# Optimization experiments

Measured on AMD Instinct MI355X. Metric: run time of the kernel, lower is better.

Reference implementation:

```python
import jax, jax.numpy as jnp
import numpy as np

B, S, U = 64, 64, 16
EMB = 10
D = U - 2 + 2 * EMB      # encoder d_model = 34
DD = 3                   # decoder d_model
FF = 4                   # dim_feedforward
NL = 4                   # num layers (enc and dec)
ENH = 2                  # encoder heads
WV, SV = 10000, 400      # word / syllable vocab sizes


def _ln(x, w, b, eps=1e-5):
    mu = jnp.mean(x, -1, keepdims=True)
    var = jnp.mean((x - mu) ** 2, -1, keepdims=True)
    return (x - mu) / jnp.sqrt(var + eps) * w + b


def _mha(xq, xkv, qkv_w, qkv_b, out_w, out_b, nhead, mask=None):
    d = xq.shape[-1]
    wq, wk, wv = jnp.split(qkv_w, 3, axis=0)
    bq, bk, bv = jnp.split(qkv_b, 3, axis=0)
    q = xq @ wq.T + bq
    k = xkv @ wk.T + bk
    v = xkv @ wv.T + bv
    b_, sq, sk = q.shape[0], q.shape[1], k.shape[1]
    dh = d // nhead
    q = q.reshape(b_, sq, nhead, dh)
    k = k.reshape(b_, sk, nhead, dh)
    v = v.reshape(b_, sk, nhead, dh)
    scores = jnp.einsum('bqhd,bkhd->bhqk', q, k) * (1.0 / np.sqrt(dh))
    if mask is not None:
        scores = scores + mask
    attn = jax.nn.softmax(scores, axis=-1)
    out = jnp.einsum('bhqk,bkhd->bqhd', attn, v).reshape(b_, sq, d)
    return out @ out_w.T + out_b


def _pos_encoding(batch, d_model):
    # Faithful to the original quirk: pe has shape [max_len, 1, d] and is added
    # to a batch-first [B,S,D] tensor as x + pe[:B]  ->  row b of pe is added
    # to ALL sequence positions of batch element b.
    pos = jnp.arange(batch, dtype=jnp.float32)[:, None]
    div = jnp.exp(jnp.arange(0, d_model, 2, dtype=jnp.float32) * (-np.log(10000.0) / d_model))
    ang = pos * div  # [B, D/2]
    pe = jnp.stack([jnp.sin(ang), jnp.cos(ang)], axis=-1).reshape(batch, d_model)
    return pe[:, None, :]  # [B,1,D]


def setup_inputs() -> dict:
    key = jax.random.key(0)
    ks = iter(jax.random.split(key, 64))

    def n(shape, s=0.1):
        return jax.random.normal(next(ks), shape, dtype=jnp.float32) * s

    base = jax.random.uniform(next(ks), (B, S, U), dtype=jnp.float32)
    widx = jax.random.randint(next(ks), (B, S), 0, WV).astype(jnp.float32)
    sidx = jax.random.randint(next(ks), (B, S), 0, SV).astype(jnp.float32)
    src = base.at[:, :, U - 2].set(widx).at[:, :, U - 1].set(sidx)
    return {
        'src': src,
        'word_emb': jax.random.uniform(next(ks), (WV, EMB), jnp.float32, -0.1, 0.1),
        'syll_emb': jax.random.uniform(next(ks), (SV, EMB), jnp.float32, -0.1, 0.1),
        'enc_qkv_w': n((NL, 3 * D, D)), 'enc_qkv_b': jnp.zeros((NL, 3 * D)),
        'enc_out_w': n((NL, D, D)), 'enc_out_b': jnp.zeros((NL, D)),
        'enc_ln1_w': jnp.ones((NL, D)), 'enc_ln1_b': jnp.zeros((NL, D)),
        'enc_lin1_w': n((NL, FF, D)), 'enc_lin1_b': jnp.zeros((NL, FF)),
        'enc_lin2_w': n((NL, D, FF)), 'enc_lin2_b': jnp.zeros((NL, D)),
        'enc_ln2_w': jnp.ones((NL, D)), 'enc_ln2_b': jnp.zeros((NL, D)),
        'norm_w': jnp.ones((D,)), 'norm_b': jnp.zeros((D,)),
        'eo_w': jax.random.uniform(next(ks), (DD, D), jnp.float32, -0.1, 0.1),
        'eo_b': jnp.zeros((DD,)),
        'dec_sa_qkv_w': n((NL, 3 * DD, DD)), 'dec_sa_qkv_b': jnp.zeros((NL, 3 * DD)),
        'dec_sa_out_w': n((NL, DD, DD)), 'dec_sa_out_b': jnp.zeros((NL, DD)),
        'dec_ln1_w': jnp.ones((NL, DD)), 'dec_ln1_b': jnp.zeros((NL, DD)),
        'dec_ca_qkv_w': n((NL, 3 * DD, DD)), 'dec_ca_qkv_b': jnp.zeros((NL, 3 * DD)),
        'dec_ca_out_w': n((NL, DD, DD)), 'dec_ca_out_b': jnp.zeros((NL, DD)),
        'dec_ln2_w': jnp.ones((NL, DD)), 'dec_ln2_b': jnp.zeros((NL, DD)),
        'dec_lin1_w': n((NL, FF, DD)), 'dec_lin1_b': jnp.zeros((NL, FF)),
        'dec_lin2_w': n((NL, DD, FF)), 'dec_lin2_b': jnp.zeros((NL, DD)),
        'dec_ln3_w': jnp.ones((NL, DD)), 'dec_ln3_b': jnp.zeros((NL, DD)),
    }


def reference(src, word_emb, syll_emb,
              enc_qkv_w, enc_qkv_b, enc_out_w, enc_out_b,
              enc_ln1_w, enc_ln1_b, enc_lin1_w, enc_lin1_b,
              enc_lin2_w, enc_lin2_b, enc_ln2_w, enc_ln2_b,
              norm_w, norm_b, eo_w, eo_b,
              dec_sa_qkv_w, dec_sa_qkv_b, dec_sa_out_w, dec_sa_out_b,
              dec_ln1_w, dec_ln1_b,
              dec_ca_qkv_w, dec_ca_qkv_b, dec_ca_out_w, dec_ca_out_b,
              dec_ln2_w, dec_ln2_b,
              dec_lin1_w, dec_lin1_b, dec_lin2_w, dec_lin2_b,
              dec_ln3_w, dec_ln3_b):
    b, s = src.shape[0], src.shape[1]
    # embed_lyrics
    widx = src[:, :, U - 2].astype(jnp.int32)
    sidx = src[:, :, U - 1].astype(jnp.int32)
    x = jnp.concatenate([src[:, :, :U - 2], word_emb[widx], syll_emb[sidx]], axis=2)  # [B,S,D]
    x = x + _pos_encoding(b, D)
    # TransformerEncoder (post-norm, relu, dropout=0) + final LayerNorm
    for l in range(NL):
        sa = _mha(x, x, enc_qkv_w[l], enc_qkv_b[l], enc_out_w[l], enc_out_b[l], ENH)
        x = _ln(x + sa, enc_ln1_w[l], enc_ln1_b[l])
        ff = jax.nn.relu(x @ enc_lin1_w[l].T + enc_lin1_b[l]) @ enc_lin2_w[l].T + enc_lin2_b[l]
        x = _ln(x + ff, enc_ln2_w[l], enc_ln2_b[l])
    x = _ln(x, norm_w, norm_b)
    memory = x @ eo_w.T + eo_b  # [B,S,3]

    causal = jnp.where(jnp.tril(jnp.ones((s, s), bool)), 0.0, -1e9).astype(jnp.float32)

    def decode(tgt):
        y = tgt
        for l in range(NL):
            sa = _mha(y, y, dec_sa_qkv_w[l], dec_sa_qkv_b[l], dec_sa_out_w[l], dec_sa_out_b[l], 1, causal)
            y = _ln(y + sa, dec_ln1_w[l], dec_ln1_b[l])
            ca = _mha(y, memory, dec_ca_qkv_w[l], dec_ca_qkv_b[l], dec_ca_out_w[l], dec_ca_out_b[l], 1)
            y = _ln(y + ca, dec_ln2_w[l], dec_ln2_b[l])
            ff = jax.nn.relu(y @ dec_lin1_w[l].T + dec_lin1_b[l]) @ dec_lin2_w[l].T + dec_lin2_b[l]
            y = _ln(y + ff, dec_ln3_w[l], dec_ln3_b[l])
        return y

    # mask, position i only depends on tgt[:, :i+1], so a fixed-size padded
    # buffer + scan computes identical values.
    def step(tgt, i):
        out_i = jax.lax.dynamic_slice_in_dim(decode(tgt), i, 1, axis=1)  # [B,1,3]
        return jax.lax.dynamic_update_slice(tgt, out_i, (0, i + 1, 0)), None

    tgt0 = jnp.zeros((b, s, DD), jnp.float32)
    tgt, _ = jax.lax.scan(step, tgt0, jnp.arange(s - 1))
    return jnp.concatenate([tgt, src[:, :, U - 2:U - 1], src[:, :, U - 1:U]], axis=2)
```

## Files before the change

kernel.cpp:

```cpp
#include <hip/hip_runtime.h>
#include <math.h>

#define B_ 64
#define S_ 64
#define U_ 16
#define EMB_ 10
#define D_ 34
#define DD_ 3
#define FF_ 4
#define NL_ 4

typedef float v2f __attribute__((ext_vector_type(2)));

__global__ __launch_bounds__(512) void enc_kernel(
    const float* __restrict__ src, const float* __restrict__ wemb,
    const float* __restrict__ semb,
    const float* __restrict__ qkv_w, const float* __restrict__ qkv_b,
    const float* __restrict__ out_w, const float* __restrict__ out_b,
    const float* __restrict__ ln1_w, const float* __restrict__ ln1_b,
    const float* __restrict__ lin1_w, const float* __restrict__ lin1_b,
    const float* __restrict__ lin2_w, const float* __restrict__ lin2_b,
    const float* __restrict__ ln2_w, const float* __restrict__ ln2_b,
    const float* __restrict__ norm_w, const float* __restrict__ norm_b,
    const float* __restrict__ eo_w, const float* __restrict__ eo_b,
    float* __restrict__ mem, float* __restrict__ out)
{
    const int b = blockIdx.x;
    const int tid = threadIdx.x;
    const int wv_ = tid >> 6;
    const int lane = tid & 63;

    __shared__ float xs[S_][D_ + 1];
    __shared__ float tmp[S_][D_ + 1];
    __shared__ float att[S_][D_ + 1];
    __shared__ __align__(16) float qsh[2][S_][21];
    __shared__ __align__(16) float ksh[2][S_][20];
    __shared__ __align__(16) float vsh[2][S_][20];
    __shared__ float ffh[S_][5];
    __shared__ float pacc[4][128][19];

    const float rs17 = 0.24253562503633297f;
    const float negln = -logf(10000.0f) / (float)D_;

    #pragma unroll
    for (int rr = 0; rr < 5; ++rr) {
        int idx = tid + rr * 512;
        if (idx < S_ * D_) {
            int pos = idx / D_, d = idx % D_;
            float v;
            if (d < U_ - 2) {
                v = src[(b * S_ + pos) * U_ + d];
            } else if (d < U_ - 2 + EMB_) {
                int wi = (int)src[(b * S_ + pos) * U_ + (U_ - 2)];
                v = wemb[wi * EMB_ + (d - (U_ - 2))];
            } else {
                int si = (int)src[(b * S_ + pos) * U_ + (U_ - 1)];
                v = semb[si * EMB_ + (d - (U_ - 2 + EMB_))];
            }
            int k = d >> 1;
            float div = __expf((float)(2 * k) * negln);
            float ang = (float)b * div;
            v += (d & 1) ? __cosf(ang) : __sinf(ang);
            xs[pos][d] = v;
        }
    }
    __syncthreads();

    for (int l = 0; l < NL_; ++l) {
        const float* Wq = qkv_w + l * 3 * D_ * D_;
        const float* Bq = qkv_b + l * 3 * D_;

        {
            v2f xr2[17];
            #pragma unroll
            for (int d2 = 0; d2 < 17; ++d2) {
                v2f t; t.x = xs[lane][2 * d2]; t.y = xs[lane][2 * d2 + 1];
                xr2[d2] = t;
            }
            #pragma unroll
            for (int rb = 0; rb < 13; ++rb) {
                int r = wv_ + (rb << 3);
                if (r < 3 * D_) {
                    int ru = __builtin_amdgcn_readfirstlane(r);
                    const v2f* w2 = (const v2f*)(Wq + ru * D_);
                    v2f a2; a2.x = Bq[ru]; a2.y = 0.f;
                    #pragma unroll
                    for (int d2 = 0; d2 < 17; ++d2)
                        a2 = __builtin_elementwise_fma(xr2[d2], w2[d2], a2);
                    float acc = a2.x + a2.y;
                    if (ru < D_)          { int h = (ru >= 17), dd = ru - h * 17; qsh[h][lane][dd] = acc; }
                    else if (ru < 2 * D_) { int rr2 = ru - D_;     int h = (rr2 >= 17), dd = rr2 - h * 17; ksh[h][lane][dd] = acc; }
                    else                  { int rr2 = ru - 2 * D_; int h = (rr2 >= 17), dd = rr2 - h * 17; vsh[h][lane][dd] = acc; }
                }
            }
        }
        __syncthreads();

        {
            int c = tid >> 7, hq = tid & 127;
            int h = hq >> 6, qi = hq & 63;
            float qv[17], acc[17];
            #pragma unroll
            for (int d = 0; d < 17; ++d) { qv[d] = qsh[h][qi][d]; acc[d] = 0.f; }
            float ssum = 0.f;
            int j0 = c * 16;
            #pragma unroll 4
            for (int jj = 0; jj < 16; ++jj) {
                int j = j0 + jj;
                const float4* kr = (const float4*)ksh[h][j];
                const float4* vr = (const float4*)vsh[h][j];
                float4 k0 = kr[0], k1 = kr[1], k2 = kr[2], k3 = kr[3];
                float  k16 = ksh[h][j][16];
                float4 v0 = vr[0], v1 = vr[1], v2 = vr[2], v3 = vr[3];
                float  v16 = vsh[h][j][16];
                float sE = qv[0]*k0.x + qv[2]*k0.z + qv[4]*k1.x + qv[6]*k1.z +
                           qv[8]*k2.x + qv[10]*k2.z + qv[12]*k3.x + qv[14]*k3.z;
                float sO = qv[1]*k0.y + qv[3]*k0.w + qv[5]*k1.y + qv[7]*k1.w +
                           qv[9]*k2.y + qv[11]*k2.w + qv[13]*k3.y + qv[15]*k3.w;
                float sc = sE + sO + qv[16]*k16;
                float e = __expf(sc * rs17);
                ssum += e;
                acc[0] += e*v0.x;  acc[1] += e*v0.y;  acc[2] += e*v0.z;  acc[3] += e*v0.w;
                acc[4] += e*v1.x;  acc[5] += e*v1.y;  acc[6] += e*v1.z;  acc[7] += e*v1.w;
                acc[8] += e*v2.x;  acc[9] += e*v2.y;  acc[10] += e*v2.z; acc[11] += e*v2.w;
                acc[12] += e*v3.x; acc[13] += e*v3.y; acc[14] += e*v3.z; acc[15] += e*v3.w;
                acc[16] += e*v16;
            }
            #pragma unroll
            for (int d = 0; d < 17; ++d) pacc[c][hq][d] = acc[d];
            pacc[c][hq][17] = ssum;
        }
        __syncthreads();

        if (tid < 128) {
            int h = tid >> 6, qi = tid & 63;
            int off = h * 17;
            float ssum = pacc[0][tid][17] + pacc[1][tid][17] +
                         pacc[2][tid][17] + pacc[3][tid][17];
            float inv = 1.f / ssum;
            #pragma unroll
            for (int d = 0; d < 17; ++d)
                att[qi][off + d] = (pacc[0][tid][d] + pacc[1][tid][d] +
                                    pacc[2][tid][d] + pacc[3][tid][d]) * inv;
        }
        __syncthreads();

        {
            v2f ar2[17];
            #pragma unroll
            for (int d2 = 0; d2 < 17; ++d2) {
                v2f t; t.x = att[lane][2 * d2]; t.y = att[lane][2 * d2 + 1];
                ar2[d2] = t;
            }
            const float* Wo = out_w + l * D_ * D_;
            const float* Bo = out_b + l * D_;
            #pragma unroll
            for (int rb = 0; rb < 5; ++rb) {
                int d = wv_ + (rb << 3);
                if (d < D_) {
                    int du = __builtin_amdgcn_readfirstlane(d);
                    const v2f* w2 = (const v2f*)(Wo + du * D_);
                    v2f a2; a2.x = Bo[du]; a2.y = 0.f;
                    #pragma unroll
                    for (int d2 = 0; d2 < 17; ++d2)
                        a2 = __builtin_elementwise_fma(ar2[d2], w2[d2], a2);
                    tmp[lane][du] = xs[lane][du] + a2.x + a2.y;
                }
            }
        }
        __syncthreads();

        {
            int row = tid >> 3, sub = tid & 7;
            float s = 0.f, sq = 0.f;
            #pragma unroll
            for (int d = sub; d < D_; d += 8) { float t = tmp[row][d]; s += t; sq = fmaf(t, t, sq); }
            #pragma unroll
            for (int m = 1; m < 8; m <<= 1) { s += __shfl_xor(s, m, 8); sq += __shfl_xor(sq, m, 8); }
            float mu = s * (1.0f / D_);
            float var = fmaf(sq, 1.0f / D_, -mu * mu);
            float rstd = rsqrtf(var + 1e-5f);
            #pragma unroll
            for (int d = sub; d < D_; d += 8)
                xs[row][d] = (tmp[row][d] - mu) * rstd * ln1_w[l * D_ + d] + ln1_b[l * D_ + d];
        }
        __syncthreads();

        if (wv_ < 4) {
            int fu = __builtin_amdgcn_readfirstlane(wv_);
            const v2f* w2 = (const v2f*)(lin1_w + l * FF_ * D_ + fu * D_);
            v2f a2; a2.x = lin1_b[l * FF_ + fu]; a2.y = 0.f;
            #pragma unroll
            for (int d2 = 0; d2 < 17; ++d2) {
                v2f t; t.x = xs[lane][2 * d2]; t.y = xs[lane][2 * d2 + 1];
                a2 = __builtin_elementwise_fma(t, w2[d2], a2);
            }
            ffh[lane][fu] = fmaxf(a2.x + a2.y, 0.f);
        }
        __syncthreads();

        {
            float h0 = ffh[lane][0], h1 = ffh[lane][1],
                  h2 = ffh[lane][2], h3 = ffh[lane][3];
            const float* W2 = lin2_w + l * D_ * FF_;
            const float* B2 = lin2_b + l * D_;
            #pragma unroll
            for (int rb = 0; rb < 5; ++rb) {
                int d = wv_ + (rb << 3);
                if (d < D_) {
                    int du = __builtin_amdgcn_readfirstlane(d);
                    const float* wrow = W2 + du * FF_;
                    float acc = fmaf(h0, wrow[0], fmaf(h1, wrow[1],
                                fmaf(h2, wrow[2], fmaf(h3, wrow[3], B2[du]))));
                    tmp[lane][du] = xs[lane][du] + acc;
                }
            }
        }
        __syncthreads();

        {
            int row = tid >> 3, sub = tid & 7;
            float s = 0.f, sq = 0.f;
            #pragma unroll
            for (int d = sub; d < D_; d += 8) { float t = tmp[row][d]; s += t; sq = fmaf(t, t, sq); }
            #pragma unroll
            for (int m = 1; m < 8; m <<= 1) { s += __shfl_xor(s, m, 8); sq += __shfl_xor(sq, m, 8); }
            float mu = s * (1.0f / D_);
            float var = fmaf(sq, 1.0f / D_, -mu * mu);
            float rstd = rsqrtf(var + 1e-5f);
            #pragma unroll
            for (int d = sub; d < D_; d += 8)
                xs[row][d] = (tmp[row][d] - mu) * rstd * ln2_w[l * D_ + d] + ln2_b[l * D_ + d];
        }
        __syncthreads();
    }

    {
        int row = tid >> 3, sub = tid & 7;
        float s = 0.f, sq = 0.f;
        #pragma unroll
        for (int d = sub; d < D_; d += 8) { float t = xs[row][d]; s += t; sq = fmaf(t, t, sq); }
        #pragma unroll
        for (int m = 1; m < 8; m <<= 1) { s += __shfl_xor(s, m, 8); sq += __shfl_xor(sq, m, 8); }
        float mu = s * (1.0f / D_);
        float var = fmaf(sq, 1.0f / D_, -mu * mu);
        float rstd = rsqrtf(var + 1e-5f);
        #pragma unroll
        for (int d = sub; d < D_; d += 8)
            tmp[row][d] = (xs[row][d] - mu) * rstd * norm_w[d] + norm_b[d];
    }
    __syncthreads();

    if (wv_ < 3) {
        int ru = __builtin_amdgcn_readfirstlane(wv_);
        const v2f* w2 = (const v2f*)(eo_w + ru * D_);
        v2f a2; a2.x = eo_b[ru]; a2.y = 0.f;
        #pragma unroll
        for (int d2 = 0; d2 < 17; ++d2) {
            v2f t; t.x = tmp[lane][2 * d2]; t.y = tmp[lane][2 * d2 + 1];
            a2 = __builtin_elementwise_fma(t, w2[d2], a2);
        }
        mem[(b * S_ + lane) * DD_ + ru] = a2.x + a2.y;
    }

    if (tid < S_) {
        out[(b * S_ + tid) * 5 + 3] = src[(b * S_ + tid) * U_ + (U_ - 2)];
        out[(b * S_ + tid) * 5 + 4] = src[(b * S_ + tid) * U_ + (U_ - 1)];
    }
}

#define PIN(x) asm volatile("" : "+v"(x))

template <int CTRL>
__device__ __forceinline__ float dpp_add(float v) {
    int t = __builtin_amdgcn_update_dpp(0, __float_as_int(v), CTRL, 0xf, 0xf, true);
    return v + __int_as_float(t);
}

__device__ __forceinline__ float wave_sum_l63(float v) {
    v = dpp_add<0x111>(v);
    v = dpp_add<0x112>(v);
    v = dpp_add<0x114>(v);
    v = dpp_add<0x118>(v);
    v = dpp_add<0x142>(v);
    v = dpp_add<0x143>(v);
    return v;
}

__device__ __forceinline__ float bcast63(float v) {
    return __int_as_float(__builtin_amdgcn_readlane(__float_as_int(v), 63));
}

__device__ __forceinline__ void ln3e(float z0, float z1, float z2,
                                     float w0, float w1, float w2,
                                     float b0, float b1, float b2,
                                     float& o0, float& o1, float& o2) {
    float s1 = (z0 + z1) + z2;
    float s2 = fmaf(z0, z0, fmaf(z1, z1, z2 * z2));
    float mu = s1 * (1.0f / 3.0f);
    float vpe = fmaf(s2, (1.0f / 3.0f), fmaf(-mu, mu, 1e-5f));
    float rstd = __builtin_amdgcn_rsqf(vpe);
    o0 = fmaf(z0 - mu, rstd * w0, b0);
    o1 = fmaf(z1 - mu, rstd * w1, b1);
    o2 = fmaf(z2 - mu, rstd * w2, b2);
}

__global__ __launch_bounds__(64, 1) void dec_kernel(
    const float* __restrict__ mem,
    const float* __restrict__ sa_qkv_w, const float* __restrict__ sa_qkv_b,
    const float* __restrict__ sa_out_w, const float* __restrict__ sa_out_b,
    const float* __restrict__ gln1_w, const float* __restrict__ gln1_b,
    const float* __restrict__ ca_qkv_w, const float* __restrict__ ca_qkv_b,
    const float* __restrict__ ca_out_w, const float* __restrict__ ca_out_b,
    const float* __restrict__ gln2_w, const float* __restrict__ gln2_b,
    const float* __restrict__ l1_w, const float* __restrict__ l1_b,
    const float* __restrict__ l2_w, const float* __restrict__ l2_b,
    const float* __restrict__ gln3_w, const float* __restrict__ gln3_b,
    float* __restrict__ out)
{
    const int b = blockIdx.x;
    const int lane = threadIdx.x;
    const float LOG2E = 1.4426950408889634f;
    const float rs3 = 0.5773502691896258f;
    const float QS = rs3 * LOG2E;

    __shared__ __align__(16) float fst[NL_][40];
    for (int t = lane; t < NL_ * 40; t += 64) {
        int l = t / 40, s = t % 40;
        float v = 0.f;
        if      (s < 12) v = l1_w[l * 12 + s];
        else if (s < 16) v = l1_b[l * 4 + (s - 12)];
        else if (s < 28) v = l2_w[l * 12 + (s - 16)];
        else if (s < 31) v = l2_b[l * 3 + (s - 28)];
        else if (s < 34) v = gln3_w[l * 3 + (s - 31)];
        else if (s < 37) v = gln3_b[l * 3 + (s - 34)];
        fst[l][s] = v;
    }
    __syncthreads();

    float Wsq[NL_][9][3], Bsq[NL_][9];
    float Wso[NL_][3][3], Bso[NL_][3];
    float N1w[NL_][3], N1b[NL_][3];
    float Wcq[NL_][3][3], Bcq[NL_][3];
    float Wco[NL_][3][3], Bco[NL_][3];
    float N2w[NL_][3], N2b[NL_][3];

    #pragma unroll
    for (int l = 0; l < NL_; ++l) {
        #pragma unroll
        for (int r = 0; r < 9; ++r) {
            float sc = (r < 3) ? QS : 1.0f;
            Bsq[l][r] = sa_qkv_b[l * 9 + r] * sc;
            #pragma unroll
            for (int c = 0; c < 3; ++c) Wsq[l][r][c] = sa_qkv_w[l * 27 + r * 3 + c] * sc;
        }
        #pragma unroll
        for (int r = 0; r < 3; ++r) {
            Bso[l][r] = sa_out_b[l * 3 + r];
            Bcq[l][r] = ca_qkv_b[l * 9 + r] * QS;
            Bco[l][r] = ca_out_b[l * 3 + r];
            N1w[l][r] = gln1_w[l * 3 + r];  N1b[l][r] = gln1_b[l * 3 + r];
            N2w[l][r] = gln2_w[l * 3 + r];  N2b[l][r] = gln2_b[l * 3 + r];
            #pragma unroll
            for (int c = 0; c < 3; ++c) {
                Wso[l][r][c] = sa_out_w[l * 9 + r * 3 + c];
                Wcq[l][r][c] = ca_qkv_w[l * 27 + r * 3 + c] * QS;
                Wco[l][r][c] = ca_out_w[l * 9 + r * 3 + c];
            }
        }
    }

    float m0 = mem[(b * S_ + lane) * DD_ + 0];
    float m1 = mem[(b * S_ + lane) * DD_ + 1];
    float m2 = mem[(b * S_ + lane) * DD_ + 2];

    float ck[NL_][3], cv[NL_][3];
    #pragma unroll
    for (int l = 0; l < NL_; ++l) {
        #pragma unroll
        for (int r = 0; r < 3; ++r) {
            ck[l][r] = ca_qkv_w[l * 27 + (3 + r) * 3 + 0] * m0 +
                       ca_qkv_w[l * 27 + (3 + r) * 3 + 1] * m1 +
                       ca_qkv_w[l * 27 + (3 + r) * 3 + 2] * m2 + ca_qkv_b[l * 9 + 3 + r];
            cv[l][r] = ca_qkv_w[l * 27 + (6 + r) * 3 + 0] * m0 +
                       ca_qkv_w[l * 27 + (6 + r) * 3 + 1] * m1 +
                       ca_qkv_w[l * 27 + (6 + r) * 3 + 2] * m2 + ca_qkv_b[l * 9 + 6 + r];
        }
    }

    #pragma unroll
    for (int l = 0; l < NL_; ++l) {
        #pragma unroll
        for (int r = 0; r < 9; ++r) {
            PIN(Bsq[l][r]);
            #pragma unroll
            for (int c = 0; c < 3; ++c) PIN(Wsq[l][r][c]);
        }
        #pragma unroll
        for (int r = 0; r < 3; ++r) {
            PIN(Bso[l][r]); PIN(Bcq[l][r]); PIN(Bco[l][r]);
            PIN(N1w[l][r]); PIN(N1b[l][r]); PIN(N2w[l][r]); PIN(N2b[l][r]);
            #pragma unroll
            for (int c = 0; c < 3; ++c) { PIN(Wso[l][r][c]); PIN(Wcq[l][r][c]); PIN(Wco[l][r][c]); }
        }
    }

    float sk[NL_][3] = {{0.f}}, sv[NL_][3] = {{0.f}};

    if (lane < 3) out[(b * S_ + 0) * 5 + lane] = 0.f;

    float y0 = 0.f, y1 = 0.f, y2 = 0.f;

    for (int i = 0; i < S_ - 1; ++i) {
        float msa = (lane <= i) ? 0.f : -1.0e30f;
        #pragma unroll
        for (int l = 0; l < NL_; ++l) {
            float wv[40];
            {
                const float4* fp = (const float4*)fst[l];
                #pragma unroll
                for (int k = 0; k < 10; ++k) {
                    float4 t4 = fp[k];
                    wv[4 * k + 0] = t4.x; wv[4 * k + 1] = t4.y;
                    wv[4 * k + 2] = t4.z; wv[4 * k + 3] = t4.w;
                }
                #pragma unroll
                for (int k = 0; k < 37; ++k) PIN(wv[k]);
            }

            float q[3], kn[3], vn[3];
            #pragma unroll
            for (int r = 0; r < 3; ++r) {
                q[r]  = fmaf(Wsq[l][r][0], y0, fmaf(Wsq[l][r][1], y1, fmaf(Wsq[l][r][2], y2, Bsq[l][r])));
                kn[r] = fmaf(Wsq[l][3 + r][0], y0, fmaf(Wsq[l][3 + r][1], y1, fmaf(Wsq[l][3 + r][2], y2, Bsq[l][3 + r])));
                vn[r] = fmaf(Wsq[l][6 + r][0], y0, fmaf(Wsq[l][6 + r][1], y1, fmaf(Wsq[l][6 + r][2], y2, Bsq[l][6 + r])));
            }
            if (lane == i) {
                #pragma unroll
                for (int r = 0; r < 3; ++r) { sk[l][r] = kn[r]; sv[l][r] = vn[r]; }
            }
            float sc = fmaf(q[0], sk[l][0], fmaf(q[1], sk[l][1], fmaf(q[2], sk[l][2], msa)));
            float e = __builtin_amdgcn_exp2f(sc);
            float es  = wave_sum_l63(e);
            float ev0 = wave_sum_l63(e * sv[l][0]);
            float ev1 = wave_sum_l63(e * sv[l][1]);
            float ev2 = wave_sum_l63(e * sv[l][2]);
            float inv = __builtin_amdgcn_rcpf(bcast63(es));
            float a0 = bcast63(ev0) * inv, a1 = bcast63(ev1) * inv, a2 = bcast63(ev2) * inv;
            float s0 = fmaf(Wso[l][0][0], a0, fmaf(Wso[l][0][1], a1, fmaf(Wso[l][0][2], a2, Bso[l][0])));
            float s1 = fmaf(Wso[l][1][0], a0, fmaf(Wso[l][1][1], a1, fmaf(Wso[l][1][2], a2, Bso[l][1])));
            float s2 = fmaf(Wso[l][2][0], a0, fmaf(Wso[l][2][1], a1, fmaf(Wso[l][2][2], a2, Bso[l][2])));
            ln3e(y0 + s0, y1 + s1, y2 + s2,
                 N1w[l][0], N1w[l][1], N1w[l][2], N1b[l][0], N1b[l][1], N1b[l][2],
                 y0, y1, y2);

            float p0 = fmaf(Wcq[l][0][0], y0, fmaf(Wcq[l][0][1], y1, fmaf(Wcq[l][0][2], y2, Bcq[l][0])));
            float p1 = fmaf(Wcq[l][1][0], y0, fmaf(Wcq[l][1][1], y1, fmaf(Wcq[l][1][2], y2, Bcq[l][1])));
            float p2 = fmaf(Wcq[l][2][0], y0, fmaf(Wcq[l][2][1], y1, fmaf(Wcq[l][2][2], y2, Bcq[l][2])));
            float sc2 = fmaf(p0, ck[l][0], fmaf(p1, ck[l][1], p2 * ck[l][2]));
            float e2 = __builtin_amdgcn_exp2f(sc2);
            float cs  = wave_sum_l63(e2);
            float cw0 = wave_sum_l63(e2 * cv[l][0]);
            float cw1 = wave_sum_l63(e2 * cv[l][1]);
            float cw2 = wave_sum_l63(e2 * cv[l][2]);
            inv = __builtin_amdgcn_rcpf(bcast63(cs));
            a0 = bcast63(cw0) * inv; a1 = bcast63(cw1) * inv; a2 = bcast63(cw2) * inv;
            float c0 = fmaf(Wco[l][0][0], a0, fmaf(Wco[l][0][1], a1, fmaf(Wco[l][0][2], a2, Bco[l][0])));
            float c1 = fmaf(Wco[l][1][0], a0, fmaf(Wco[l][1][1], a1, fmaf(Wco[l][1][2], a2, Bco[l][1])));
            float c2 = fmaf(Wco[l][2][0], a0, fmaf(Wco[l][2][1], a1, fmaf(Wco[l][2][2], a2, Bco[l][2])));
            ln3e(y0 + c0, y1 + c1, y2 + c2,
                 N2w[l][0], N2w[l][1], N2w[l][2], N2b[l][0], N2b[l][1], N2b[l][2],
                 y0, y1, y2);

            float h0 = fmaxf(fmaf(wv[0], y0, fmaf(wv[1],  y1, fmaf(wv[2],  y2, wv[12]))), 0.f);
            float h1 = fmaxf(fmaf(wv[3], y0, fmaf(wv[4],  y1, fmaf(wv[5],  y2, wv[13]))), 0.f);
            float h2 = fmaxf(fmaf(wv[6], y0, fmaf(wv[7],  y1, fmaf(wv[8],  y2, wv[14]))), 0.f);
            float h3 = fmaxf(fmaf(wv[9], y0, fmaf(wv[10], y1, fmaf(wv[11], y2, wv[15]))), 0.f);
            float f0 = fmaf(wv[16], h0, fmaf(wv[17], h1, fmaf(wv[18], h2, fmaf(wv[19], h3, wv[28]))));
            float f1 = fmaf(wv[20], h0, fmaf(wv[21], h1, fmaf(wv[22], h2, fmaf(wv[23], h3, wv[29]))));
            float f2 = fmaf(wv[24], h0, fmaf(wv[25], h1, fmaf(wv[26], h2, fmaf(wv[27], h3, wv[30]))));
            ln3e(y0 + f0, y1 + f1, y2 + f2,
                 wv[31], wv[32], wv[33], wv[34], wv[35], wv[36],
                 y0, y1, y2);
        }
        if (lane == 0) {
            out[(b * S_ + i + 1) * 5 + 0] = y0;
            out[(b * S_ + i + 1) * 5 + 1] = y1;
            out[(b * S_ + i + 1) * 5 + 2] = y2;
        }
    }
}

extern "C" void kernel_launch(void* const* d_in, const int* in_sizes, int n_in,
                              void* d_out, int out_size, void* d_ws, size_t ws_size,
                              hipStream_t stream) {
    const float* src  = (const float*)d_in[0];
    const float* wemb = (const float*)d_in[1];
    const float* semb = (const float*)d_in[2];

    float* mem = (float*)d_ws;
    float* out = (float*)d_out;

    enc_kernel<<<B_, 512, 0, stream>>>(
        src, wemb, semb,
        (const float*)d_in[3],  (const float*)d_in[4],
        (const float*)d_in[5],  (const float*)d_in[6],
        (const float*)d_in[7],  (const float*)d_in[8],
        (const float*)d_in[9],  (const float*)d_in[10],
        (const float*)d_in[11], (const float*)d_in[12],
        (const float*)d_in[13], (const float*)d_in[14],
        (const float*)d_in[15], (const float*)d_in[16],
        (const float*)d_in[17], (const float*)d_in[18],
        mem, out);

    dec_kernel<<<B_, 64, 0, stream>>>(
        mem,
        (const float*)d_in[19], (const float*)d_in[20],
        (const float*)d_in[21], (const float*)d_in[22],
        (const float*)d_in[23], (const float*)d_in[24],
        (const float*)d_in[25], (const float*)d_in[26],
        (const float*)d_in[27], (const float*)d_in[28],
        (const float*)d_in[29], (const float*)d_in[30],
        (const float*)d_in[31], (const float*)d_in[32],
        (const float*)d_in[33], (const float*)d_in[34],
        (const float*)d_in[35], (const float*)d_in[36],
        out);
}
```

Baseline: 335.4 us.

## Fold attention projections into precomputed keys/values and shorten causal reductions

The decoder's cross-attention query projection is folded into precomputed per-lane key vectors (cu, cb), and the output projection is folded into the value vectors (cvp), so each step skips two 3x3 matvecs. Self-attention values are stored already multiplied by the output projection. The causal self-attention reduction now runs only the 16-lane DPP stages when fewer lanes are active, adding the row-crossing stages only once i passes 15 or 31. Biases are added into the residual early to shorten the dependency chain. Because the projections are reassociated, floating-point rounding changes slightly, and the uniform branches on i add a little control flow.

```diff
diff --git a/kernel.cpp b/kernel.cpp
--- a/kernel.cpp
+++ b/kernel.cpp
@@ -277,18 +277,16 @@
     return v + __int_as_float(t);
 }
 
-__device__ __forceinline__ float wave_sum_l63(float v) {
+__device__ __forceinline__ float red16(float v) {
     v = dpp_add<0x111>(v);
     v = dpp_add<0x112>(v);
     v = dpp_add<0x114>(v);
     v = dpp_add<0x118>(v);
-    v = dpp_add<0x142>(v);
-    v = dpp_add<0x143>(v);
     return v;
 }
 
-__device__ __forceinline__ float bcast63(float v) {
-    return __int_as_float(__builtin_amdgcn_readlane(__float_as_int(v), 63));
+__device__ __forceinline__ float rlane(float v, int l) {
+    return __int_as_float(__builtin_amdgcn_readlane(__float_as_int(v), l));
 }
 
 __device__ __forceinline__ void ln3e(float z0, float z1, float z2,
@@ -341,9 +339,11 @@
     float Wsq[NL_][9][3], Bsq[NL_][9];
     float Wso[NL_][3][3], Bso[NL_][3];
     float N1w[NL_][3], N1b[NL_][3];
-    float Wcq[NL_][3][3], Bcq[NL_][3];
-    float Wco[NL_][3][3], Bco[NL_][3];
     float N2w[NL_][3], N2b[NL_][3];
+    float Bco[NL_][3];
+    float cu[NL_][3];
+    float cb[NL_];
+    float cvp[NL_][3];
 
     #pragma unroll
     for (int l = 0; l < NL_; ++l) {
@@ -357,16 +357,11 @@
         #pragma unroll
         for (int r = 0; r < 3; ++r) {
             Bso[l][r] = sa_out_b[l * 3 + r];
-            Bcq[l][r] = ca_qkv_b[l * 9 + r] * QS;
             Bco[l][r] = ca_out_b[l * 3 + r];
             N1w[l][r] = gln1_w[l * 3 + r];  N1b[l][r] = gln1_b[l * 3 + r];
             N2w[l][r] = gln2_w[l * 3 + r];  N2b[l][r] = gln2_b[l * 3 + r];
             #pragma unroll
-            for (int c = 0; c < 3; ++c) {
-                Wso[l][r][c] = sa_out_w[l * 9 + r * 3 + c];
-                Wcq[l][r][c] = ca_qkv_w[l * 27 + r * 3 + c] * QS;
-                Wco[l][r][c] = ca_out_w[l * 9 + r * 3 + c];
-            }
+            for (int c = 0; c < 3; ++c) Wso[l][r][c] = sa_out_w[l * 9 + r * 3 + c];
         }
     }
 
@@ -374,18 +369,31 @@
     float m1 = mem[(b * S_ + lane) * DD_ + 1];
     float m2 = mem[(b * S_ + lane) * DD_ + 2];
 
-    float ck[NL_][3], cv[NL_][3];
     #pragma unroll
     for (int l = 0; l < NL_; ++l) {
+        float ck[3], cv[3];
         #pragma unroll
         for (int r = 0; r < 3; ++r) {
-            ck[l][r] = ca_qkv_w[l * 27 + (3 + r) * 3 + 0] * m0 +
-                       ca_qkv_w[l * 27 + (3 + r) * 3 + 1] * m1 +
-                       ca_qkv_w[l * 27 + (3 + r) * 3 + 2] * m2 + ca_qkv_b[l * 9 + 3 + r];
-            cv[l][r] = ca_qkv_w[l * 27 + (6 + r) * 3 + 0] * m0 +
-                       ca_qkv_w[l * 27 + (6 + r) * 3 + 1] * m1 +
-                       ca_qkv_w[l * 27 + (6 + r) * 3 + 2] * m2 + ca_qkv_b[l * 9 + 6 + r];
-        }
+            ck[r] = ca_qkv_w[l * 27 + (3 + r) * 3 + 0] * m0 +
+                    ca_qkv_w[l * 27 + (3 + r) * 3 + 1] * m1 +
+                    ca_qkv_w[l * 27 + (3 + r) * 3 + 2] * m2 + ca_qkv_b[l * 9 + 3 + r];
+            cv[r] = ca_qkv_w[l * 27 + (6 + r) * 3 + 0] * m0 +
+                    ca_qkv_w[l * 27 + (6 + r) * 3 + 1] * m1 +
+                    ca_qkv_w[l * 27 + (6 + r) * 3 + 2] * m2 + ca_qkv_b[l * 9 + 6 + r];
+        }
+        #pragma unroll
+        for (int s = 0; s < 3; ++s)
+            cu[l][s] = QS * (ca_qkv_w[l * 27 + 0 + s] * ck[0] +
+                             ca_qkv_w[l * 27 + 3 + s] * ck[1] +
+                             ca_qkv_w[l * 27 + 6 + s] * ck[2]);
+        cb[l] = QS * (ca_qkv_b[l * 9 + 0] * ck[0] +
+                      ca_qkv_b[l * 9 + 1] * ck[1] +
+                      ca_qkv_b[l * 9 + 2] * ck[2]);
+        #pragma unroll
+        for (int r = 0; r < 3; ++r)
+            cvp[l][r] = ca_out_w[l * 9 + r * 3 + 0] * cv[0] +
+                        ca_out_w[l * 9 + r * 3 + 1] * cv[1] +
+                        ca_out_w[l * 9 + r * 3 + 2] * cv[2];
     }
 
     #pragma unroll
@@ -396,12 +404,14 @@
             #pragma unroll
             for (int c = 0; c < 3; ++c) PIN(Wsq[l][r][c]);
         }
+        PIN(cb[l]);
         #pragma unroll
         for (int r = 0; r < 3; ++r) {
-            PIN(Bso[l][r]); PIN(Bcq[l][r]); PIN(Bco[l][r]);
+            PIN(Bso[l][r]); PIN(Bco[l][r]);
             PIN(N1w[l][r]); PIN(N1b[l][r]); PIN(N2w[l][r]); PIN(N2b[l][r]);
-            #pragma unroll
-            for (int c = 0; c < 3; ++c) { PIN(Wso[l][r][c]); PIN(Wcq[l][r][c]); PIN(Wco[l][r][c]); }
+            PIN(cu[l][r]);  PIN(cvp[l][r]);
+            #pragma unroll
+            for (int c = 0; c < 3; ++c) PIN(Wso[l][r][c]);
         }
     }
 
@@ -424,62 +434,76 @@
                     wv[4 * k + 0] = t4.x; wv[4 * k + 1] = t4.y;
                     wv[4 * k + 2] = t4.z; wv[4 * k + 3] = t4.w;
                 }
-                #pragma unroll
-                for (int k = 0; k < 37; ++k) PIN(wv[k]);
-            }
-
-            float q[3], kn[3], vn[3];
+            }
+
+            float q[3], kn[3], vn[3], vp[3];
             #pragma unroll
             for (int r = 0; r < 3; ++r) {
+                kn[r] = fmaf(Wsq[l][3 + r][0], y0, fmaf(Wsq[l][3 + r][1], y1, fmaf(Wsq[l][3 + r][2], y2, Bsq[l][3 + r])));
                 q[r]  = fmaf(Wsq[l][r][0], y0, fmaf(Wsq[l][r][1], y1, fmaf(Wsq[l][r][2], y2, Bsq[l][r])));
-                kn[r] = fmaf(Wsq[l][3 + r][0], y0, fmaf(Wsq[l][3 + r][1], y1, fmaf(Wsq[l][3 + r][2], y2, Bsq[l][3 + r])));
                 vn[r] = fmaf(Wsq[l][6 + r][0], y0, fmaf(Wsq[l][6 + r][1], y1, fmaf(Wsq[l][6 + r][2], y2, Bsq[l][6 + r])));
             }
+            #pragma unroll
+            for (int r = 0; r < 3; ++r)
+                vp[r] = fmaf(Wso[l][r][0], vn[0], fmaf(Wso[l][r][1], vn[1], Wso[l][r][2] * vn[2]));
             if (lane == i) {
                 #pragma unroll
-                for (int r = 0; r < 3; ++r) { sk[l][r] = kn[r]; sv[l][r] = vn[r]; }
+                for (int r = 0; r < 3; ++r) { sk[l][r] = kn[r]; sv[l][r] = vp[r]; }
             }
             float sc = fmaf(q[0], sk[l][0], fmaf(q[1], sk[l][1], fmaf(q[2], sk[l][2], msa)));
             float e = __builtin_amdgcn_exp2f(sc);
-            float es  = wave_sum_l63(e);
-            float ev0 = wave_sum_l63(e * sv[l][0]);
-            float ev1 = wave_sum_l63(e * sv[l][1]);
-            float ev2 = wave_sum_l63(e * sv[l][2]);
-            float inv = __builtin_amdgcn_rcpf(bcast63(es));
-            float a0 = bcast63(ev0) * inv, a1 = bcast63(ev1) * inv, a2 = bcast63(ev2) * inv;
-            float s0 = fmaf(Wso[l][0][0], a0, fmaf(Wso[l][0][1], a1, fmaf(Wso[l][0][2], a2, Bso[l][0])));
-            float s1 = fmaf(Wso[l][1][0], a0, fmaf(Wso[l][1][1], a1, fmaf(Wso[l][1][2], a2, Bso[l][1])));
-            float s2 = fmaf(Wso[l][2][0], a0, fmaf(Wso[l][2][1], a1, fmaf(Wso[l][2][2], a2, Bso[l][2])));
-            ln3e(y0 + s0, y1 + s1, y2 + s2,
+            float se  = red16(e);
+            float sa0 = red16(e * sv[l][0]);
+            float sa1 = red16(e * sv[l][1]);
+            float sa2 = red16(e * sv[l][2]);
+            int rl = 15;
+            if (i >= 15) {
+                se  = dpp_add<0x142>(se);  sa0 = dpp_add<0x142>(sa0);
+                sa1 = dpp_add<0x142>(sa1); sa2 = dpp_add<0x142>(sa2);
+                rl = 31;
+            }
+            if (i >= 31) {
+                se  = dpp_add<0x143>(se);  sa0 = dpp_add<0x143>(sa0);
+                sa1 = dpp_add<0x143>(sa1); sa2 = dpp_add<0x143>(sa2);
+                rl = 63;
+            }
+            float yb0 = y0 + Bso[l][0], yb1 = y1 + Bso[l][1], yb2 = y2 + Bso[l][2];
+            float es = rlane(se, rl);
+            float S0 = rlane(sa0, rl), S1 = rlane(sa1, rl), S2 = rlane(sa2, rl);
+            float inv = __builtin_amdgcn_rcpf(es);
+            ln3e(fmaf(S0, inv, yb0), fmaf(S1, inv, yb1), fmaf(S2, inv, yb2),
                  N1w[l][0], N1w[l][1], N1w[l][2], N1b[l][0], N1b[l][1], N1b[l][2],
                  y0, y1, y2);
 
-            float p0 = fmaf(Wcq[l][0][0], y0, fmaf(Wcq[l][0][1], y1, fmaf(Wcq[l][0][2], y2, Bcq[l][0])));
-            float p1 = fmaf(Wcq[l][1][0], y0, fmaf(Wcq[l][1][1], y1, fmaf(Wcq[l][1][2], y2, Bcq[l][1])));
-            float p2 = fmaf(Wcq[l][2][0], y0, fmaf(Wcq[l][2][1], y1, fmaf(Wcq[l][2][2], y2, Bcq[l][2])));
-            float sc2 = fmaf(p0, ck[l][0], fmaf(p1, ck[l][1], p2 * ck[l][2]));
+            float sc2 = fmaf(y0, cu[l][0], fmaf(y1, cu[l][1], fmaf(y2, cu[l][2], cb[l])));
             float e2 = __builtin_amdgcn_exp2f(sc2);
-            float cs  = wave_sum_l63(e2);
-            float cw0 = wave_sum_l63(e2 * cv[l][0]);
-            float cw1 = wave_sum_l63(e2 * cv[l][1]);
-            float cw2 = wave_sum_l63(e2 * cv[l][2]);
-            inv = __builtin_amdgcn_rcpf(bcast63(cs));
-            a0 = bcast63(cw0) * inv; a1 = bcast63(cw1) * inv; a2 = bcast63(cw2) * inv;
-            float c0 = fmaf(Wco[l][0][0], a0, fmaf(Wco[l][0][1], a1, fmaf(Wco[l][0][2], a2, Bco[l][0])));
-            float c1 = fmaf(Wco[l][1][0], a0, fmaf(Wco[l][1][1], a1, fmaf(Wco[l][1][2], a2, Bco[l][1])));
-            float c2 = fmaf(Wco[l][2][0], a0, fmaf(Wco[l][2][1], a1, fmaf(Wco[l][2][2], a2, Bco[l][2])));
-            ln3e(y0 + c0, y1 + c1, y2 + c2,
+            float ce  = red16(e2);
+            float ca0 = red16(e2 * cvp[l][0]);
+            float ca1 = red16(e2 * cvp[l][1]);
+            float ca2 = red16(e2 * cvp[l][2]);
+            ce  = dpp_add<0x142>(ce);  ca0 = dpp_add<0x142>(ca0);
+            ca1 = dpp_add<0x142>(ca1); ca2 = dpp_add<0x142>(ca2);
+            ce  = dpp_add<0x143>(ce);  ca0 = dpp_add<0x143>(ca0);
+            ca1 = dpp_add<0x143>(ca1); ca2 = dpp_add<0x143>(ca2);
+            float yc0 = y0 + Bco[l][0], yc1 = y1 + Bco[l][1], yc2 = y2 + Bco[l][2];
+            float cs = rlane(ce, 63);
+            float C0 = rlane(ca0, 63), C1 = rlane(ca1, 63), C2 = rlane(ca2, 63);
+            float inv2 = __builtin_amdgcn_rcpf(cs);
+            ln3e(fmaf(C0, inv2, yc0), fmaf(C1, inv2, yc1), fmaf(C2, inv2, yc2),
                  N2w[l][0], N2w[l][1], N2w[l][2], N2b[l][0], N2b[l][1], N2b[l][2],
                  y0, y1, y2);
 
+            #pragma unroll
+            for (int k = 0; k < 37; ++k) PIN(wv[k]);
             float h0 = fmaxf(fmaf(wv[0], y0, fmaf(wv[1],  y1, fmaf(wv[2],  y2, wv[12]))), 0.f);
             float h1 = fmaxf(fmaf(wv[3], y0, fmaf(wv[4],  y1, fmaf(wv[5],  y2, wv[13]))), 0.f);
             float h2 = fmaxf(fmaf(wv[6], y0, fmaf(wv[7],  y1, fmaf(wv[8],  y2, wv[14]))), 0.f);
             float h3 = fmaxf(fmaf(wv[9], y0, fmaf(wv[10], y1, fmaf(wv[11], y2, wv[15]))), 0.f);
-            float f0 = fmaf(wv[16], h0, fmaf(wv[17], h1, fmaf(wv[18], h2, fmaf(wv[19], h3, wv[28]))));
-            float f1 = fmaf(wv[20], h0, fmaf(wv[21], h1, fmaf(wv[22], h2, fmaf(wv[23], h3, wv[29]))));
-            float f2 = fmaf(wv[24], h0, fmaf(wv[25], h1, fmaf(wv[26], h2, fmaf(wv[27], h3, wv[30]))));
-            ln3e(y0 + f0, y1 + f1, y2 + f2,
+            float yf0 = y0 + wv[28], yf1 = y1 + wv[29], yf2 = y2 + wv[30];
+            float f0 = fmaf(wv[16], h0, fmaf(wv[17], h1, fmaf(wv[18], h2, fmaf(wv[19], h3, yf0))));
+            float f1 = fmaf(wv[20], h0, fmaf(wv[21], h1, fmaf(wv[22], h2, fmaf(wv[23], h3, yf1))));
+            float f2 = fmaf(wv[24], h0, fmaf(wv[25], h1, fmaf(wv[26], h2, fmaf(wv[27], h3, yf2))));
+            ln3e(f0, f1, f2,
                  wv[31], wv[32], wv[33], wv[34], wv[35], wv[36],
                  y0, y1, y2);
         }
```

Measured after the change: 327.3 us. -2.4%, faster.
